# Optimization experiments

Measured on AMD Instinct MI355X. Metric: run time of the kernel, lower is better.

The kernel has to match this reference:

```python
import jax, jax.numpy as jnp
import numpy as np
import math

NB_STEPS = 50          # quadrature sub-intervals -> 51 Clenshaw-Curtis points
NUM_RNN_STEPS = 2


def _cc_weights(nb_steps):
    # Faithful port of UMNN's compute_cc_weights (Clenshaw-Curtis quadrature).
    lam = np.arange(0, nb_steps + 1).reshape(-1, 1).astype(np.float64)
    lam = np.cos((lam @ lam.T) * math.pi / nb_steps)
    lam[:, 0] = 0.5
    lam[:, -1] = 0.5 * lam[:, -1]
    lam = lam * 2.0 / nb_steps
    W = np.arange(0, nb_steps + 1).reshape(-1, 1).astype(np.float64)
    W[np.arange(1, nb_steps + 1, 2)] = 0
    W = 2.0 / (1.0 - W ** 2)
    W[0] = 1.0
    W[np.arange(1, nb_steps + 1, 2)] = 0
    cc = (lam.T @ W).astype(np.float32).reshape(-1)                      # [S]
    steps = np.cos(np.arange(0, nb_steps + 1) * math.pi / nb_steps).astype(np.float32)  # [S]
    return jnp.asarray(cc), jnp.asarray(steps)

CC_W, CC_STEPS = _cc_weights(NB_STEPS)  # S = NB_STEPS + 1 = 51


def _integrand(t, h, W1, b1, W2, b2, W3, b3, final_w):
    # IntegrandNN: MLP(cat(t,h)) -> ELU + 1 (>=0) -> fused power features -> ReLU(Linear)
    z = jnp.concatenate([t, h], axis=1)          # [N, in_d]
    z = jax.nn.relu(z @ W1.T + b1)               # [N, 128]
    z = jax.nn.relu(z @ W2.T + b2)               # [N, 128]
    z = jax.nn.elu(z @ W3.T + b3) + 1.0          # [N, 1], >= 0
    p = jnp.concatenate([z ** 1.5, z ** 2, z ** 2.5, z ** 3, z ** 3.5], axis=1)  # [N, 5]
    return jax.nn.relu((1.0 / (p + 1.0)) @ final_w.T)  # [N, 1]


def _inner_integral(x, h, params):
    # InnerUMNN: integral of IntegrandNN from x to xmax, xmax = max(x) + 10 (global scalar)
    N = x.shape[0]
    S = NB_STEPS + 1
    xmax = jnp.max(x) + 10.0
    T = x + (xmax - x) * (CC_STEPS[None, :] + 1.0) * 0.5   # [N, S]
    Tf = T.reshape(N * S, 1)
    hf = jnp.broadcast_to(h[:, None, :], (N, S, h.shape[1])).reshape(N * S, -1)
    g = _integrand(Tf, hf, *params).reshape(N, S)
    z = jnp.sum(g * CC_W[None, :], axis=1, keepdims=True)  # [N, 1]
    return z * (xmax - x) * 0.5


def _outer_integral(xT, h, params):
    # ParallelNeuralIntegral of InnerUMNN from x0 = 0 to xT; xT: [B, 1]
    B = xT.shape[0]
    S = NB_STEPS + 1
    X = xT * (CC_STEPS[None, :] + 1.0) * 0.5               # [B, S] (x0 = 0)
    Xf = X.reshape(B * S, 1)
    hf = jnp.broadcast_to(h[:, None, :], (B, S, h.shape[1])).reshape(B * S, -1)
    f = _inner_integral(Xf, hf, params).reshape(B, S)      # nested quadrature
    z = jnp.sum(f * CC_W[None, :], axis=1, keepdims=True)  # [B, 1]
    return z * xT * 0.5


def setup_inputs() -> dict:
    key = jax.random.key(0)
    ks = jax.random.split(key, 8)
    B, NF, IN_D, H = 256, 512, 64, 128
    x_ = jax.random.normal(ks[0], (B, NF), jnp.float32)
    h_ = jax.random.normal(ks[1], (B, IN_D - 1), jnp.float32)

    def lin(k, o, i):
        lim = 1.0 / np.sqrt(i)
        kw, kb = jax.random.split(k)
        return (jax.random.uniform(kw, (o, i), jnp.float32, -lim, lim),
                jax.random.uniform(kb, (o,), jnp.float32, -lim, lim))

    W1, b1 = lin(ks[2], H, IN_D)
    W2, b2 = lin(ks[3], H, H)
    W3, b3 = lin(ks[4], 1, H)
    lim5 = 1.0 / np.sqrt(5.0)
    final_w = jnp.abs(jax.random.uniform(ks[5], (1, 5), jnp.float32, -lim5, lim5))  # reset_params: abs
    log_weight = jnp.ones((1, NF), jnp.float32)            # reset_parameters: all ones
    sigmoid_param = jax.random.normal(ks[6], (1,), jnp.float32)
    return dict(x_=x_, h_=h_, W1=W1, b1=b1, W2=W2, b2=b2, W3=W3, b3=b3,
                final_w=final_w, log_weight=log_weight, sigmoid_param=sigmoid_param)


def reference(x_, h_, W1, b1, W2, b2, W3, b3, final_w, log_weight, sigmoid_param):
    params = (W1, b1, W2, b2, W3, b3, final_w)
    # compute_modular_function: F.linear then sum over dim 1 -> [B, 1]
    xm = jnp.sum(x_ @ log_weight.T, axis=1, keepdims=True)
    lam = jax.nn.sigmoid(sigmoid_param)                    # [1]
    out = jnp.zeros_like(xm)
    for _ in range(NUM_RNN_STEPS):
        xT = (1.0 - lam) * xm + lam * out
        out = _outer_integral(xT, h_, params)
    return out
```

## Files before the change

### kernel.cpp

```cpp
#include <hip/hip_runtime.h>
#include <math.h>

#define BB 256
#define NF 512
#define IND 64
#define HD 128
#define SS 51
#define NHM1 63

#define WS_LAM  0
#define WS_CCW  16
#define WS_U    80
#define WS_XM   144
#define WS_OUT1 656
#define WSH_C1  2048
#define WSH_W1  34816
#define WSH_W2F 40960
#define WS_W2F_F4 5120

typedef _Float16 f16x2 __attribute__((ext_vector_type(2)));
typedef __fp16   fp16x2 __attribute__((ext_vector_type(2)));
typedef _Float16 f16x8 __attribute__((ext_vector_type(8)));
typedef float    f32x16 __attribute__((ext_vector_type(16)));

union f16x8_split { f16x8 v8; f16x2 v2[4]; };
union pk_cast { fp16x2 p; f16x2 f; };

static __device__ inline f16x2 cvt_pk(float a, float b) {
    pk_cast u; u.p = __builtin_amdgcn_cvt_pkrtz(a, b);
    return u.f;
}

static __device__ inline float dot2f(f16x2 a, f16x2 b, float c) {
#if __has_builtin(__builtin_amdgcn_fdot2)
    return __builtin_amdgcn_fdot2(a, b, c, false);
#else
    return c + (float)a[0] * (float)b[0] + (float)a[1] * (float)b[1];
#endif
}

__global__ void k_setup(const float* __restrict__ x_, const float* __restrict__ h_,
                        const float* __restrict__ W1, const float* __restrict__ b1,
                        const float* __restrict__ W2, const float* __restrict__ lw,
                        const float* __restrict__ sp, float* __restrict__ ws) {
    int b = blockIdx.x;
    int j = threadIdx.x;
    short* wsh = (short*)ws;

    float acc = b1[j];
    const float* w1row = W1 + j * IND;
    const float* hrow  = h_ + b * NHM1;
    #pragma unroll 7
    for (int k = 0; k < NHM1; ++k) acc = fmaf(w1row[1 + k], hrow[k], acc);
    {
        _Float16 hv = (_Float16)acc;
        short sv; __builtin_memcpy(&sv, &hv, 2);
        wsh[WSH_C1 + b * HD + j] = sv;
    }

    float s = 0.f;
    for (int k = j; k < NF; k += HD) s = fmaf(x_[b * NF + k], lw[k], s);
    __shared__ float red[HD];
    red[j] = s;
    __syncthreads();
    for (int off = 64; off > 0; off >>= 1) {
        if (j < off) red[j] += red[j + off];
        __syncthreads();
    }
    if (j == 0) ws[WS_XM + b] = red[0];

    if (b < 128) {
        int d = b * 128 + j;
        int i = d & 7, lane = (d >> 3) & 63, kn = d >> 9;
        int kk = kn >> 2, nt = kn & 3;
        int row = nt * 32 + (lane & 31);
        int k = kk * 16 + (lane >> 5) * 8 + i;
        _Float16 hv = (_Float16)W2[row * HD + k];
        short sv; __builtin_memcpy(&sv, &hv, 2);
        wsh[WSH_W2F + d] = sv;
    }

    if (b == 0) {
        if (j < SS) {
            float acc2 = 0.f;
            for (int jj = 0; jj <= 50; jj += 2) {
                float wj = (jj == 0) ? 1.f : 2.f / (1.f - (float)(jj * jj));
                float lamv;
                if (j == 0 || j == 50) {
                    lamv = 0.02f;
                } else {
                    int m = (jj * j) % 100;
                    lamv = cosf((float)m * (float)M_PI / 50.f) * 0.04f;
                }
                acc2 = fmaf(lamv, wj, acc2);
            }
            ws[WS_CCW + j] = acc2;
            float st = cosf((float)j * (float)M_PI / 50.f);
            ws[WS_U + j] = (st + 1.f) * 0.5f;
        }
        if (j == 127) ws[WS_LAM] = 1.f / (1.f + expf(-sp[0]));
    }
    if (b == 2) {
        _Float16 hv = (_Float16)W1[j * IND];
        short sv; __builtin_memcpy(&sv, &hv, 2);
        wsh[WSH_W1 + j] = sv;
    }
    if (b == 4) ws[WS_OUT1 + j] = 0.f;
    if (b == 5) ws[WS_OUT1 + 128 + j] = 0.f;
}

__launch_bounds__(256, 2)
__global__ void k_int(const float* __restrict__ b2, const float* __restrict__ W3,
                      const float* __restrict__ b3, const float* __restrict__ fw,
                      const float* __restrict__ ws, const float* __restrict__ outprev,
                      float* __restrict__ tgt, float* __restrict__ ztgt) {
    int b = blockIdx.x >> 1, hf = blockIdx.x & 1;
    int tid = threadIdx.x;
    int wv = tid >> 6, l = tid & 63;
    int e32 = l & 31, h2 = l >> 5;

    __shared__ __align__(16) short w2s[16384];
    __shared__ __align__(16) short c1h[HD], w1h[HD];
    __shared__ float us[SS], ccs[SS], xw[4];

    if (ztgt && hf == 0 && tid == 0) ztgt[b] = 0.f;

    {
        const float4* src = reinterpret_cast<const float4*>(ws) + WS_W2F_F4;
        float4* dst = reinterpret_cast<float4*>(w2s);
        #pragma unroll
        for (int k = 0; k < 8; ++k) dst[tid + k * 256] = src[tid + k * 256];
    }
    {
        const short* wsh0 = (const short*)ws;
        if (tid < HD) { c1h[tid] = wsh0[WSH_C1 + b * HD + tid]; w1h[tid] = wsh0[WSH_W1 + tid]; }
    }
    if (tid < SS) { us[tid] = ws[WS_U + tid]; ccs[tid] = ws[WS_CCW + tid]; }

    float lam = ws[WS_LAM];
    float xmv = ws[WS_XM + tid];
    float opv = outprev ? outprev[tid] : 0.f;
    float xtv = (1.f - lam) * xmv + lam * opv;
    float mx = fmaxf(xtv, 0.f);
    #pragma unroll
    for (int off = 32; off >= 1; off >>= 1) mx = fmaxf(mx, __shfl_xor(mx, off, 64));
    if (l == 0) xw[wv] = mx;
    __syncthreads();
    float xmax = fmaxf(fmaxf(xw[0], xw[1]), fmaxf(xw[2], xw[3])) + 10.f;
    float xT = (1.f - lam) * ws[WS_XM + b] + lam * (outprev ? outprev[b] : 0.f);

    f16x2 b2pk[4][8], w3pk[4][8];
    #pragma unroll
    for (int nt = 0; nt < 4; ++nt) {
        int jb = nt * 32;
        #pragma unroll
        for (int q = 0; q < 8; ++q) {
            int r0 = ((2 * q) & 3) + 8 * ((2 * q) >> 2) + 4 * h2;
            b2pk[nt][q] = cvt_pk(b2[jb + r0], b2[jb + r0 + 1]);
            w3pk[nt][q] = cvt_pk(W3[jb + r0], W3[jb + r0 + 1]);
        }
    }
    float b3v = b3[0];
    float fw0 = fw[0], fw1 = fw[1], fw2 = fw[2], fw3 = fw[3], fw4 = fw[4];

    float accO = 0.f;
    float zsA = 0.f, wA = 0.f, zsB = 0.f, wB = 0.f;
    const f16x2 z2 = {(_Float16)0.f, (_Float16)0.f};

    #pragma unroll 1
    for (int d = 0; d < 6; ++d) {
        float t0, t1, ws0, ws1;
        #pragma unroll
        for (int p = 0; p < 2; ++p) {
            int tl = hf * 4 + wv + (2 * d + p) * 8;
            int m = tl * 32 + e32;
            int valid = (m <= 2600);
            int mm = valid ? m : 2600;
            int s  = (mm * 41121) >> 21;
            int si = mm - s * 51;
            float x = xT * us[s];
            float range = xmax - x;
            float t = fmaf(range, us[si], x);
            float wgt = valid ? (ccs[si] * ccs[s] * range * xT * 0.25f) : 0.f;
            float wsel = h2 ? 0.f : wgt;
            if (p == 0) { t0 = t; ws0 = wsel; } else { t1 = t; ws1 = wsel; }
        }
        _Float16 th0 = (_Float16)t0, th1 = (_Float16)t1;
        f16x2 tv0 = {th0, th0}, tv1 = {th1, th1};

        f32x16 C0, C1, C2, C3, C4, C5, C6, C7;
        #pragma unroll
        for (int e = 0; e < 16; ++e) {
            C0[e] = 0.f; C1[e] = 0.f; C2[e] = 0.f; C3[e] = 0.f;
            C4[e] = 0.f; C5[e] = 0.f; C6[e] = 0.f; C7[e] = 0.f;
        }

        {
            float z = zsA > 0.f ? zsA + 1.f : __expf(zsA);
            float sq = sqrtf(z);
            float p15 = z * sq, p2 = z * z, p25 = p2 * sq, p3 = p2 * z, p35 = p3 * sq;
            float g = fw0 * __builtin_amdgcn_rcpf(p15 + 1.f)
                    + fw1 * __builtin_amdgcn_rcpf(p2  + 1.f)
                    + fw2 * __builtin_amdgcn_rcpf(p25 + 1.f)
                    + fw3 * __builtin_amdgcn_rcpf(p3  + 1.f)
                    + fw4 * __builtin_amdgcn_rcpf(p35 + 1.f);
            accO = fmaf(fmaxf(g, 0.f), wA, accO);
            z = zsB > 0.f ? zsB + 1.f : __expf(zsB);
            sq = sqrtf(z);
            p15 = z * sq; p2 = z * z; p25 = p2 * sq; p3 = p2 * z; p35 = p3 * sq;
            g = fw0 * __builtin_amdgcn_rcpf(p15 + 1.f)
              + fw1 * __builtin_amdgcn_rcpf(p2  + 1.f)
              + fw2 * __builtin_amdgcn_rcpf(p25 + 1.f)
              + fw3 * __builtin_amdgcn_rcpf(p3  + 1.f)
              + fw4 * __builtin_amdgcn_rcpf(p35 + 1.f);
            accO = fmaf(fmaxf(g, 0.f), wB, accO);
        }

        #pragma unroll
        for (int kp = 0; kp < 4; ++kp) {
            __builtin_amdgcn_sched_barrier(0);
            #pragma unroll
            for (int kd = 0; kd < 2; ++kd) {
                int kk = kp * 2 + kd;
                f16x8_split c8, w8, Bu0, Bu1;
                c8.v8 = *reinterpret_cast<const f16x8*>(&c1h[kk * 16 + h2 * 8]);
                w8.v8 = *reinterpret_cast<const f16x8*>(&w1h[kk * 16 + h2 * 8]);
                #pragma unroll
                for (int p = 0; p < 4; ++p) {
                    Bu0.v2[p] = __builtin_elementwise_max(
                        __builtin_elementwise_fma(w8.v2[p], tv0, c8.v2[p]), z2);
                    Bu1.v2[p] = __builtin_elementwise_max(
                        __builtin_elementwise_fma(w8.v2[p], tv1, c8.v2[p]), z2);
                }
                const f16x8* Afp = reinterpret_cast<const f16x8*>(
                    &w2s[(kk * 4 * 64 + l) * 8]);
                f16x8 A0 = Afp[0], A1 = Afp[64], A2 = Afp[128], A3 = Afp[192];
                C0 = __builtin_amdgcn_mfma_f32_32x32x16_f16(A0, Bu0.v8, C0, 0, 0, 0);
                C4 = __builtin_amdgcn_mfma_f32_32x32x16_f16(A0, Bu1.v8, C4, 0, 0, 0);
                C1 = __builtin_amdgcn_mfma_f32_32x32x16_f16(A1, Bu0.v8, C1, 0, 0, 0);
                C5 = __builtin_amdgcn_mfma_f32_32x32x16_f16(A1, Bu1.v8, C5, 0, 0, 0);
                C2 = __builtin_amdgcn_mfma_f32_32x32x16_f16(A2, Bu0.v8, C2, 0, 0, 0);
                C6 = __builtin_amdgcn_mfma_f32_32x32x16_f16(A2, Bu1.v8, C6, 0, 0, 0);
                C3 = __builtin_amdgcn_mfma_f32_32x32x16_f16(A3, Bu0.v8, C3, 0, 0, 0);
                C7 = __builtin_amdgcn_mfma_f32_32x32x16_f16(A3, Bu1.v8, C7, 0, 0, 0);
            }
        }
        __builtin_amdgcn_sched_barrier(0);

        {
            float za = 0.f, zb = 0.f, zc = 0.f, zd = 0.f;
            #pragma unroll
            for (int q = 0; q < 8; ++q) {
                f16x2 a0 = cvt_pk(C0[2 * q], C0[2 * q + 1]);
                a0 = __builtin_elementwise_max(a0 + b2pk[0][q], z2);
                za = dot2f(a0, w3pk[0][q], za);
                f16x2 a1 = cvt_pk(C1[2 * q], C1[2 * q + 1]);
                a1 = __builtin_elementwise_max(a1 + b2pk[1][q], z2);
                zb = dot2f(a1, w3pk[1][q], zb);
                f16x2 a2 = cvt_pk(C2[2 * q], C2[2 * q + 1]);
                a2 = __builtin_elementwise_max(a2 + b2pk[2][q], z2);
                zc = dot2f(a2, w3pk[2][q], zc);
                f16x2 a3 = cvt_pk(C3[2 * q], C3[2 * q + 1]);
                a3 = __builtin_elementwise_max(a3 + b2pk[3][q], z2);
                zd = dot2f(a3, w3pk[3][q], zd);
            }
            float z1 = (za + zb) + (zc + zd);
            z1 += __shfl_xor(z1, 32, 64);
            zsA = z1 + b3v;
            wA = ws0;
        }
        {
            float za = 0.f, zb = 0.f, zc = 0.f, zd = 0.f;
            #pragma unroll
            for (int q = 0; q < 8; ++q) {
                f16x2 a0 = cvt_pk(C4[2 * q], C4[2 * q + 1]);
                a0 = __builtin_elementwise_max(a0 + b2pk[0][q], z2);
                za = dot2f(a0, w3pk[0][q], za);
                f16x2 a1 = cvt_pk(C5[2 * q], C5[2 * q + 1]);
                a1 = __builtin_elementwise_max(a1 + b2pk[1][q], z2);
                zb = dot2f(a1, w3pk[1][q], zb);
                f16x2 a2 = cvt_pk(C6[2 * q], C6[2 * q + 1]);
                a2 = __builtin_elementwise_max(a2 + b2pk[2][q], z2);
                zc = dot2f(a2, w3pk[2][q], zc);
                f16x2 a3 = cvt_pk(C7[2 * q], C7[2 * q + 1]);
                a3 = __builtin_elementwise_max(a3 + b2pk[3][q], z2);
                zd = dot2f(a3, w3pk[3][q], zd);
            }
            float z1 = (za + zb) + (zc + zd);
            z1 += __shfl_xor(z1, 32, 64);
            zsB = z1 + b3v;
            wB = ws1;
        }
    }

    {
        float z = zsA > 0.f ? zsA + 1.f : __expf(zsA);
        float sq = sqrtf(z);
        float p15 = z * sq, p2 = z * z, p25 = p2 * sq, p3 = p2 * z, p35 = p3 * sq;
        float g = fw0 * __builtin_amdgcn_rcpf(p15 + 1.f)
                + fw1 * __builtin_amdgcn_rcpf(p2  + 1.f)
                + fw2 * __builtin_amdgcn_rcpf(p25 + 1.f)
                + fw3 * __builtin_amdgcn_rcpf(p3  + 1.f)
                + fw4 * __builtin_amdgcn_rcpf(p35 + 1.f);
        accO = fmaf(fmaxf(g, 0.f), wA, accO);
        z = zsB > 0.f ? zsB + 1.f : __expf(zsB);
        sq = sqrtf(z);
        p15 = z * sq; p2 = z * z; p25 = p2 * sq; p3 = p2 * z; p35 = p3 * sq;
        g = fw0 * __builtin_amdgcn_rcpf(p15 + 1.f)
          + fw1 * __builtin_amdgcn_rcpf(p2  + 1.f)
          + fw2 * __builtin_amdgcn_rcpf(p25 + 1.f)
          + fw3 * __builtin_amdgcn_rcpf(p3  + 1.f)
          + fw4 * __builtin_amdgcn_rcpf(p35 + 1.f);
        accO = fmaf(fmaxf(g, 0.f), wB, accO);
    }

    #pragma unroll
    for (int off = 32; off >= 1; off >>= 1) accO += __shfl_xor(accO, off, 64);
    if (l == 0) atomicAdd(&tgt[b], accO);
}

extern "C" void kernel_launch(void* const* d_in, const int* in_sizes, int n_in,
                              void* d_out, int out_size, void* d_ws, size_t ws_size,
                              hipStream_t stream) {
    (void)in_sizes; (void)n_in; (void)out_size; (void)ws_size;
    const float* x_ = (const float*)d_in[0];
    const float* h_ = (const float*)d_in[1];
    const float* W1 = (const float*)d_in[2];
    const float* b1 = (const float*)d_in[3];
    const float* W2 = (const float*)d_in[4];
    const float* b2 = (const float*)d_in[5];
    const float* W3 = (const float*)d_in[6];
    const float* b3 = (const float*)d_in[7];
    const float* fw = (const float*)d_in[8];
    const float* lw = (const float*)d_in[9];
    const float* sp = (const float*)d_in[10];
    float* wsf  = (float*)d_ws;
    float* out1 = wsf + WS_OUT1;
    float* out  = (float*)d_out;

    k_setup<<<BB, HD, 0, stream>>>(x_, h_, W1, b1, W2, lw, sp, wsf);
    k_int<<<BB * 2, 256, 0, stream>>>(b2, W3, b3, fw, wsf, nullptr, out1, out);
    k_int<<<BB * 2, 256, 0, stream>>>(b2, W3, b3, fw, wsf, out1, out, nullptr);
}
```

Before: 74.77 us.

## Keep W2 MFMA fragments in registers and use one block per batch row

Removes the shared-memory staging of W2, c1 and w1 and instead loads each wave's W2 MFMA A-fragments and the c1/w1 packed values straight into registers once per block. The grid is halved to one block per batch element, and each wave now handles 21 tiles over 11 iterations instead of 6 iterations over half the tiles. This removes LDS traffic inside the MFMA loop and the duplicated W2 staging per half-block. In exchange it adds heavy register pressure (128 VGPRs for A-fragments plus accumulators), lowers launch bounds to one block per SIMD set, and leaves 256 blocks that may underfill the CUs.

```diff
diff --git a/kernel.cpp b/kernel.cpp
--- a/kernel.cpp
+++ b/kernel.cpp
@@ -16,7 +16,6 @@
 #define WSH_C1  2048
 #define WSH_W1  34816
 #define WSH_W2F 40960
-#define WS_W2F_F4 5120
 
 typedef _Float16 f16x2 __attribute__((ext_vector_type(2)));
 typedef __fp16   fp16x2 __attribute__((ext_vector_type(2)));
@@ -109,32 +108,19 @@
     if (b == 5) ws[WS_OUT1 + 128 + j] = 0.f;
 }
 
-__launch_bounds__(256, 2)
+__launch_bounds__(256, 1)
 __global__ void k_int(const float* __restrict__ b2, const float* __restrict__ W3,
                       const float* __restrict__ b3, const float* __restrict__ fw,
                       const float* __restrict__ ws, const float* __restrict__ outprev,
                       float* __restrict__ tgt, float* __restrict__ ztgt) {
-    int b = blockIdx.x >> 1, hf = blockIdx.x & 1;
+    int b = blockIdx.x;
     int tid = threadIdx.x;
     int wv = tid >> 6, l = tid & 63;
     int e32 = l & 31, h2 = l >> 5;
 
-    __shared__ __align__(16) short w2s[16384];
-    __shared__ __align__(16) short c1h[HD], w1h[HD];
     __shared__ float us[SS], ccs[SS], xw[4];
 
-    if (ztgt && hf == 0 && tid == 0) ztgt[b] = 0.f;
-
-    {
-        const float4* src = reinterpret_cast<const float4*>(ws) + WS_W2F_F4;
-        float4* dst = reinterpret_cast<float4*>(w2s);
-        #pragma unroll
-        for (int k = 0; k < 8; ++k) dst[tid + k * 256] = src[tid + k * 256];
-    }
-    {
-        const short* wsh0 = (const short*)ws;
-        if (tid < HD) { c1h[tid] = wsh0[WSH_C1 + b * HD + tid]; w1h[tid] = wsh0[WSH_W1 + tid]; }
-    }
+    if (ztgt && tid == 0) ztgt[b] = 0.f;
     if (tid < SS) { us[tid] = ws[WS_U + tid]; ccs[tid] = ws[WS_CCW + tid]; }
 
     float lam = ws[WS_LAM];
@@ -149,6 +135,26 @@
     float xmax = fmaxf(fmaxf(xw[0], xw[1]), fmaxf(xw[2], xw[3])) + 10.f;
     float xT = (1.f - lam) * ws[WS_XM + b] + lam * (outprev ? outprev[b] : 0.f);
 
+    const short* wsh = (const short*)ws;
+
+    f16x8 Af[8][4];
+    #pragma unroll
+    for (int kk = 0; kk < 8; ++kk)
+        #pragma unroll
+        for (int nt = 0; nt < 4; ++nt)
+            Af[kk][nt] = *reinterpret_cast<const f16x8*>(
+                wsh + WSH_W2F + ((kk * 4 + nt) * 64 + l) * 8);
+
+    f16x2 c1p[8][4], w1p[8][4];
+    #pragma unroll
+    for (int kk = 0; kk < 8; ++kk) {
+        f16x8_split c8, w8;
+        c8.v8 = *reinterpret_cast<const f16x8*>(wsh + WSH_C1 + b * HD + kk * 16 + h2 * 8);
+        w8.v8 = *reinterpret_cast<const f16x8*>(wsh + WSH_W1 + kk * 16 + h2 * 8);
+        #pragma unroll
+        for (int p = 0; p < 4; ++p) { c1p[kk][p] = c8.v2[p]; w1p[kk][p] = w8.v2[p]; }
+    }
+
     f16x2 b2pk[4][8], w3pk[4][8];
     #pragma unroll
     for (int nt = 0; nt < 4; ++nt) {
@@ -168,14 +174,14 @@
     const f16x2 z2 = {(_Float16)0.f, (_Float16)0.f};
 
     #pragma unroll 1
-    for (int d = 0; d < 6; ++d) {
+    for (int d = 0; d < 11; ++d) {
         float t0, t1, ws0, ws1;
         #pragma unroll
         for (int p = 0; p < 2; ++p) {
-            int tl = hf * 4 + wv + (2 * d + p) * 8;
-            int m = tl * 32 + e32;
-            int valid = (m <= 2600);
-            int mm = valid ? m : 2600;
+            int itp = 2 * d + p;
+            int m = (wv * 21 + itp) * 32 + e32;
+            int valid = (itp < 21) && (m <= 2600);
+            int mm = (m <= 2600) ? m : 2600;
             int s  = (mm * 41121) >> 21;
             int si = mm - s * 51;
             float x = xT * us[s];
@@ -217,35 +223,24 @@
         }
 
         #pragma unroll
-        for (int kp = 0; kp < 4; ++kp) {
-            __builtin_amdgcn_sched_barrier(0);
+        for (int kk = 0; kk < 8; ++kk) {
+            f16x8_split Bu0, Bu1;
             #pragma unroll
-            for (int kd = 0; kd < 2; ++kd) {
-                int kk = kp * 2 + kd;
-                f16x8_split c8, w8, Bu0, Bu1;
-                c8.v8 = *reinterpret_cast<const f16x8*>(&c1h[kk * 16 + h2 * 8]);
-                w8.v8 = *reinterpret_cast<const f16x8*>(&w1h[kk * 16 + h2 * 8]);
-                #pragma unroll
-                for (int p = 0; p < 4; ++p) {
-                    Bu0.v2[p] = __builtin_elementwise_max(
-                        __builtin_elementwise_fma(w8.v2[p], tv0, c8.v2[p]), z2);
-                    Bu1.v2[p] = __builtin_elementwise_max(
-                        __builtin_elementwise_fma(w8.v2[p], tv1, c8.v2[p]), z2);
-                }
-                const f16x8* Afp = reinterpret_cast<const f16x8*>(
-                    &w2s[(kk * 4 * 64 + l) * 8]);
-                f16x8 A0 = Afp[0], A1 = Afp[64], A2 = Afp[128], A3 = Afp[192];
-                C0 = __builtin_amdgcn_mfma_f32_32x32x16_f16(A0, Bu0.v8, C0, 0, 0, 0);
-                C4 = __builtin_amdgcn_mfma_f32_32x32x16_f16(A0, Bu1.v8, C4, 0, 0, 0);
-                C1 = __builtin_amdgcn_mfma_f32_32x32x16_f16(A1, Bu0.v8, C1, 0, 0, 0);
-                C5 = __builtin_amdgcn_mfma_f32_32x32x16_f16(A1, Bu1.v8, C5, 0, 0, 0);
-                C2 = __builtin_amdgcn_mfma_f32_32x32x16_f16(A2, Bu0.v8, C2, 0, 0, 0);
-                C6 = __builtin_amdgcn_mfma_f32_32x32x16_f16(A2, Bu1.v8, C6, 0, 0, 0);
-                C3 = __builtin_amdgcn_mfma_f32_32x32x16_f16(A3, Bu0.v8, C3, 0, 0, 0);
-                C7 = __builtin_amdgcn_mfma_f32_32x32x16_f16(A3, Bu1.v8, C7, 0, 0, 0);
+            for (int p = 0; p < 4; ++p) {
+                Bu0.v2[p] = __builtin_elementwise_max(
+                    __builtin_elementwise_fma(w1p[kk][p], tv0, c1p[kk][p]), z2);
+                Bu1.v2[p] = __builtin_elementwise_max(
+                    __builtin_elementwise_fma(w1p[kk][p], tv1, c1p[kk][p]), z2);
             }
-        }
-        __builtin_amdgcn_sched_barrier(0);
+            C0 = __builtin_amdgcn_mfma_f32_32x32x16_f16(Af[kk][0], Bu0.v8, C0, 0, 0, 0);
+            C4 = __builtin_amdgcn_mfma_f32_32x32x16_f16(Af[kk][0], Bu1.v8, C4, 0, 0, 0);
+            C1 = __builtin_amdgcn_mfma_f32_32x32x16_f16(Af[kk][1], Bu0.v8, C1, 0, 0, 0);
+            C5 = __builtin_amdgcn_mfma_f32_32x32x16_f16(Af[kk][1], Bu1.v8, C5, 0, 0, 0);
+            C2 = __builtin_amdgcn_mfma_f32_32x32x16_f16(Af[kk][2], Bu0.v8, C2, 0, 0, 0);
+            C6 = __builtin_amdgcn_mfma_f32_32x32x16_f16(Af[kk][2], Bu1.v8, C6, 0, 0, 0);
+            C3 = __builtin_amdgcn_mfma_f32_32x32x16_f16(Af[kk][3], Bu0.v8, C3, 0, 0, 0);
+            C7 = __builtin_amdgcn_mfma_f32_32x32x16_f16(Af[kk][3], Bu1.v8, C7, 0, 0, 0);
+        }
 
         {
             float za = 0.f, zb = 0.f, zc = 0.f, zd = 0.f;
@@ -339,6 +334,6 @@
     float* out  = (float*)d_out;
 
     k_setup<<<BB, HD, 0, stream>>>(x_, h_, W1, b1, W2, lw, sp, wsf);
-    k_int<<<BB * 2, 256, 0, stream>>>(b2, W3, b3, fw, wsf, nullptr, out1, out);
-    k_int<<<BB * 2, 256, 0, stream>>>(b2, W3, b3, fw, wsf, out1, out, nullptr);
-}
+    k_int<<<BB, 256, 0, stream>>>(b2, W3, b3, fw, wsf, nullptr, out1, out);
+    k_int<<<BB, 256, 0, stream>>>(b2, W3, b3, fw, wsf, out1, out, nullptr);
+}
```

Result: slower. 77.97 us (+4.3%).
